# Performance work log

Hardware: AMD Instinct MI355X
Metric: run time of the kernel (lower is better)

Reference implementation:

```python
import jax, jax.numpy as jnp
import numpy as np

IN_DIM = 768
D_MODEL = 256
B, T = 64, 2048
LN_EPS = 1e-5


def setup_inputs() -> dict:
    key = jax.random.key(0)
    ks = jax.random.split(key, 8)
    s_in = 1.0 / np.sqrt(IN_DIM)
    s_d = 1.0 / np.sqrt(D_MODEL)
    return {
        "x": jax.random.normal(ks[0], (B, T, IN_DIM), dtype=jnp.float32),
        "ln_gamma": jnp.ones((IN_DIM,), jnp.float32),
        "ln_beta": jnp.zeros((IN_DIM,), jnp.float32),
        "W_proj": jax.random.uniform(ks[1], (IN_DIM, D_MODEL), jnp.float32, -s_in, s_in),
        "b_proj": jax.random.uniform(ks[2], (D_MODEL,), jnp.float32, -s_in, s_in),
        "W1": jax.random.uniform(ks[3], (D_MODEL, D_MODEL), jnp.float32, -s_d, s_d),
        "b1": jax.random.uniform(ks[4], (D_MODEL,), jnp.float32, -s_d, s_d),
        "W2": jax.random.uniform(ks[5], (D_MODEL,), jnp.float32, -s_d, s_d),
        "b2": jax.random.uniform(ks[6], (), jnp.float32, -s_d, s_d),
    }


def reference(x, ln_gamma, ln_beta, W_proj, b_proj, W1, b1, W2, b2):
    # nan/inf sanitization to 0
    x = jnp.nan_to_num(x, nan=0.0, posinf=0.0, neginf=0.0)
    # LayerNorm over last dim (biased variance, eps=1e-5)
    mu = jnp.mean(x, axis=-1, keepdims=True)
    var = jnp.mean(jnp.square(x - mu), axis=-1, keepdims=True)
    xn = (x - mu) * jax.lax.rsqrt(var + LN_EPS) * ln_gamma + ln_beta
    # projection to d_model: [B, T, D]
    h = jnp.einsum('btf,fd->btd', xn, W_proj) + b_proj
    # tanh-MLP attention scores: [B, T]
    a = jnp.tanh(jnp.einsum('btd,de->bte', h, W1) + b1)
    w = jnp.einsum('bte,e->bt', a, W2) + b2
    w = jax.nn.softmax(w, axis=-1)
    # weighted-sum pooling over T: [B, D]
    return jnp.einsum('btd,bt->bd', h, w)
```

## Files before the change

kernel.cpp:

```cpp
#include <hip/hip_runtime.h>

#define LN_EPS 1e-5f

typedef __attribute__((ext_vector_type(8))) short s8vec;
typedef __attribute__((ext_vector_type(4))) float f4vec;

#define OFF_WPT   0u
#define OFF_W1T   393216u
#define OFF_U     524288u
#define OFF_C     525312u
#define OFF_UPART 526336u
#define OFF_VPART 575488u
#define OFF_PM    624640u
#define OFF_PS    632832u
#define OFF_PO    641024u

__device__ __forceinline__ unsigned short f2bf(float f) {
  unsigned int u = __float_as_uint(f);
  u += 0x7fffu + ((u >> 16) & 1u);
  return (unsigned short)(u >> 16);
}
__device__ __forceinline__ float bf2f(unsigned short h) {
  return __uint_as_float(((unsigned int)h) << 16);
}
__device__ __forceinline__ void gll16(const void* g, void* l) {
  __builtin_amdgcn_global_load_lds(
      (const __attribute__((address_space(1))) unsigned int*)g,
      (__attribute__((address_space(3))) unsigned int*)l, 16, 0, 0);
}

__global__ void k0_prep(const float* __restrict__ Wp,
                        const float* __restrict__ gamma,
                        const float* __restrict__ beta,
                        const float* __restrict__ W1,
                        char* __restrict__ ws) {
  const int blk = blockIdx.x;
  const int n = threadIdx.x;
  const int sw = (n & 7) << 4;
  if (blk < 48) {
    unsigned short* wpt = (unsigned short*)(ws + OFF_WPT);
    const int k0 = blk * 16;
    float up = 0.f, vp = 0.f;
#pragma unroll
    for (int j = 0; j < 16; ++j) {
      const int k = k0 + j;
      const float w = Wp[k * 256 + n];
      const float wpv = gamma[k] * w;
      up += wpv;
      vp += beta[k] * w;
      const int c = k >> 6, kc = k & 63;
      wpt[c * 16384 + n * 64 + ((((kc * 2) ^ sw)) >> 1)] = f2bf(wpv);
    }
    ((float*)(ws + OFF_UPART))[blk * 256 + n] = up;
    ((float*)(ws + OFF_VPART))[blk * 256 + n] = vp;
  } else {
    unsigned short* w1t = (unsigned short*)(ws + OFF_W1T);
    const int d0 = (blk - 48) * 16;
#pragma unroll
    for (int j = 0; j < 16; ++j) {
      const int d = d0 + j;
      const int c = d >> 6, dc = d & 63;
      w1t[c * 16384 + n * 64 + ((((dc * 2) ^ sw)) >> 1)] = f2bf(W1[d * 256 + n]);
    }
  }
}

__global__ void k0_reduce(const float* __restrict__ bproj, char* __restrict__ ws) {
  const int n = threadIdx.x;
  const float* upart = (const float*)(ws + OFF_UPART);
  const float* vpart = (const float*)(ws + OFF_VPART);
  float u = 0.f, v = 0.f;
  for (int i = 0; i < 48; ++i) {
    u += upart[i * 256 + n];
    v += vpart[i * 256 + n];
  }
  ((float*)(ws + OFF_U))[n] = u;
  ((float*)(ws + OFF_C))[n] = v + bproj[n];
}

__global__ __launch_bounds__(256, 2)
void k1_main(const float* __restrict__ x,
             const float* __restrict__ b1,
             const float* __restrict__ W2,
             char* __restrict__ ws) {
  __shared__ __align__(16) char sm_h[32768];
  __shared__ __align__(16) char sm_b[32768];
  __shared__ __align__(16) char sm_a[8192];
  __shared__ float sm_u[256], sm_c[256], sm_b1[256], sm_w2[256];
  __shared__ float sm_mu[64], sm_inv[64];
  __shared__ float sm_lp[64 * 4];
  __shared__ float sm_lg[64];
  __shared__ float sm_e[64];

  const int tid  = threadIdx.x;
  const int lane = tid & 63;
  const int wid  = tid >> 6;
  const int lr = lane & 15;
  const int lq = lane >> 4;

  sm_u[tid]  = ((const float*)(ws + OFF_U))[tid];
  sm_c[tid]  = ((const float*)(ws + OFF_C))[tid];
  sm_b1[tid] = b1[tid];
  sm_w2[tid] = W2[tid];

  const int arow = tid >> 2;
  const int aq   = tid & 3;
  const float* xrow = x + (size_t)(blockIdx.x * 64 + arow) * 768 + aq * 16;

  const char* bsrc = (const char*)ws + OFF_WPT + wid * 8192 + lane * 16;
  char*       bdst = sm_b + wid * 8192 + lane * 16;

  const f4vec fz = {0.f, 0.f, 0.f, 0.f};
  f4vec acc[4][4];
#pragma unroll
  for (int m = 0; m < 4; ++m)
#pragma unroll
    for (int n = 0; n < 4; ++n) acc[m][n] = fz;

  float s1 = 0.f, s2 = 0.f;
  float4 va[4];
#pragma unroll
  for (int j = 0; j < 4; ++j) va[j] = *(const float4*)(xrow + j * 4);

  for (int c = 0; c < 12; ++c) {
#pragma unroll
    for (int s = 0; s < 8; ++s) gll16(bsrc + c * 32768 + s * 1024, bdst + s * 1024);
    float v[16];
#pragma unroll
    for (int j = 0; j < 4; ++j) {
      v[4*j+0] = va[j].x; v[4*j+1] = va[j].y; v[4*j+2] = va[j].z; v[4*j+3] = va[j].w;
    }
    unsigned int pk[8];
#pragma unroll
    for (int j = 0; j < 16; ++j) {
      float f = v[j];
      if ((__float_as_uint(f) & 0x7f800000u) == 0x7f800000u) f = 0.f;
      s1 += f; s2 += f * f;
      const unsigned int hb = f2bf(f);
      if ((j & 1) == 0) pk[j >> 1] = hb; else pk[j >> 1] |= hb << 16;
    }
    {
      const int base = arow * 128 + aq * 32;
      const int sw = (arow & 7) << 4;
      *(int4*)(sm_a + ((base     ) ^ sw)) = make_int4((int)pk[0], (int)pk[1], (int)pk[2], (int)pk[3]);
      *(int4*)(sm_a + ((base + 16) ^ sw)) = make_int4((int)pk[4], (int)pk[5], (int)pk[6], (int)pk[7]);
    }
    if (c < 11) {
#pragma unroll
      for (int j = 0; j < 4; ++j) va[j] = *(const float4*)(xrow + (c + 1) * 64 + j * 4);
    }
    __syncthreads();
#pragma unroll
    for (int ks = 0; ks < 2; ++ks) {
      const int kb = (ks * 32 + lq * 8) * 2;
      s8vec af[4], bfv[4];
#pragma unroll
      for (int m = 0; m < 4; ++m) {
        const int row = m * 16 + lr;
        af[m] = *(const s8vec*)(sm_a + ((row * 128 + kb) ^ ((row & 7) << 4)));
      }
#pragma unroll
      for (int n = 0; n < 4; ++n) {
        const int row = wid * 64 + n * 16 + lr;
        bfv[n] = *(const s8vec*)(sm_b + ((row * 128 + kb) ^ ((row & 7) << 4)));
      }
#pragma unroll
      for (int m = 0; m < 4; ++m)
#pragma unroll
        for (int n = 0; n < 4; ++n)
          acc[m][n] = __builtin_amdgcn_mfma_f32_16x16x32_bf16(af[m], bfv[n], acc[m][n], 0, 0, 0);
    }
    __syncthreads();
  }

  s1 += __shfl_xor(s1, 1); s1 += __shfl_xor(s1, 2);
  s2 += __shfl_xor(s2, 1); s2 += __shfl_xor(s2, 2);
  if (aq == 0) {
    const float mu = s1 * (1.f / 768.f);
    float var = s2 * (1.f / 768.f) - mu * mu;
    var = fmaxf(var, 0.f);
    sm_mu[arow]  = mu;
    sm_inv[arow] = rsqrtf(var + LN_EPS);
  }
  __syncthreads();

#pragma unroll
  for (int m = 0; m < 4; ++m) {
#pragma unroll
    for (int i = 0; i < 4; ++i) {
      const int rl = m * 16 + lq * 4 + i;
      const float mu  = sm_mu[rl];
      const float inv = sm_inv[rl];
      const int sw = (rl & 7) << 4;
#pragma unroll
      for (int n = 0; n < 4; ++n) {
        const int cd = wid * 64 + n * 16 + lr;
        const float h = inv * (acc[m][n][i] - mu * sm_u[cd]) + sm_c[cd];
        *(unsigned short*)(sm_h + ((rl * 512 + cd * 2) ^ sw)) = f2bf(h);
      }
    }
  }
  __syncthreads();

  f4vec acc2[4][4];
#pragma unroll
  for (int m = 0; m < 4; ++m)
#pragma unroll
    for (int n = 0; n < 4; ++n) acc2[m][n] = fz;

  const char* b2src = (const char*)ws + OFF_W1T + wid * 8192 + lane * 16;
  for (int c = 0; c < 4; ++c) {
#pragma unroll
    for (int s = 0; s < 8; ++s) gll16(b2src + c * 32768 + s * 1024, bdst + s * 1024);
    __syncthreads();
#pragma unroll
    for (int ks = 0; ks < 2; ++ks) {
      const int kh = (c * 64 + ks * 32 + lq * 8) * 2;
      const int kb = (ks * 32 + lq * 8) * 2;
      s8vec af[4], bfv[4];
#pragma unroll
      for (int m = 0; m < 4; ++m) {
        const int row = m * 16 + lr;
        af[m] = *(const s8vec*)(sm_h + ((row * 512 + kh) ^ ((row & 7) << 4)));
      }
#pragma unroll
      for (int n = 0; n < 4; ++n) {
        const int row = wid * 64 + n * 16 + lr;
        bfv[n] = *(const s8vec*)(sm_b + ((row * 128 + kb) ^ ((row & 7) << 4)));
      }
#pragma unroll
      for (int m = 0; m < 4; ++m)
#pragma unroll
        for (int n = 0; n < 4; ++n)
          acc2[m][n] = __builtin_amdgcn_mfma_f32_16x16x32_bf16(af[m], bfv[n], acc2[m][n], 0, 0, 0);
    }
    __syncthreads();
  }

  float lp[4][4];
#pragma unroll
  for (int m = 0; m < 4; ++m)
#pragma unroll
    for (int i = 0; i < 4; ++i) lp[m][i] = 0.f;

#pragma unroll
  for (int m = 0; m < 4; ++m) {
#pragma unroll
    for (int n = 0; n < 4; ++n) {
      const int cd = wid * 64 + n * 16 + lr;
      const float b1v = sm_b1[cd];
      const float w2v = sm_w2[cd];
#pragma unroll
      for (int i = 0; i < 4; ++i) {
        float z = acc2[m][n][i] + b1v;
        z = fminf(fmaxf(z, -15.f), 15.f);
        const float e2 = __expf(2.f * z);
        const float a = (e2 - 1.f) / (e2 + 1.f);
        lp[m][i] += a * w2v;
      }
    }
  }
#pragma unroll
  for (int m = 0; m < 4; ++m) {
#pragma unroll
    for (int i = 0; i < 4; ++i) {
      float t = lp[m][i];
      t += __shfl_xor(t, 1);
      t += __shfl_xor(t, 2);
      t += __shfl_xor(t, 4);
      t += __shfl_xor(t, 8);
      if (lr == 0) sm_lp[(m * 16 + lq * 4 + i) * 4 + wid] = t;
    }
  }
  __syncthreads();
  if (tid < 64)
    sm_lg[tid] = sm_lp[tid*4+0] + sm_lp[tid*4+1] + sm_lp[tid*4+2] + sm_lp[tid*4+3];
  __syncthreads();

  float mx = -1e30f;
  for (int r = 0; r < 64; ++r) mx = fmaxf(mx, sm_lg[r]);
  if (tid < 64) sm_e[tid] = __expf(sm_lg[tid] - mx);
  __syncthreads();

  {
    const int d = tid;
    float o = 0.f;
    for (int r = 0; r < 64; ++r) {
      const float ev = sm_e[r];
      const unsigned short hb =
          *(const unsigned short*)(sm_h + ((r * 512 + d * 2) ^ ((r & 7) << 4)));
      o += ev * bf2f(hb);
    }
    ((float*)(ws + OFF_PO))[blockIdx.x * 256 + d] = o;
  }
  if (tid == 0) {
    float s = 0.f;
    for (int r = 0; r < 64; ++r) s += sm_e[r];
    ((float*)(ws + OFF_PS))[blockIdx.x] = s;
    ((float*)(ws + OFF_PM))[blockIdx.x] = mx;
  }
}

__global__ void k2_combine(const char* __restrict__ ws, float* __restrict__ out) {
  const int b = blockIdx.x;
  const int d = threadIdx.x;
  const float* pm = (const float*)(ws + OFF_PM) + b * 32;
  const float* ps = (const float*)(ws + OFF_PS) + b * 32;
  const float* po = (const float*)(ws + OFF_PO) + (size_t)b * 32 * 256;
  float mx = -1e30f;
  for (int c = 0; c < 32; ++c) mx = fmaxf(mx, pm[c]);
  float num = 0.f, den = 0.f;
  for (int c = 0; c < 32; ++c) {
    const float al = __expf(pm[c] - mx);
    den += al * ps[c];
    num += al * po[c * 256 + d];
  }
  out[b * 256 + d] = num / den;
}

extern "C" void kernel_launch(void* const* d_in, const int* in_sizes, int n_in,
                              void* d_out, int out_size, void* d_ws, size_t ws_size,
                              hipStream_t stream) {
  const float* x     = (const float*)d_in[0];
  const float* gamma = (const float*)d_in[1];
  const float* beta  = (const float*)d_in[2];
  const float* Wp    = (const float*)d_in[3];
  const float* bproj = (const float*)d_in[4];
  const float* W1    = (const float*)d_in[5];
  const float* b1    = (const float*)d_in[6];
  const float* W2    = (const float*)d_in[7];
  char* ws = (char*)d_ws;
  float* out = (float*)d_out;

  k0_prep   <<<dim3(64),   dim3(256), 0, stream>>>(Wp, gamma, beta, W1, ws);
  k0_reduce <<<dim3(1),    dim3(256), 0, stream>>>(bproj, ws);
  k1_main   <<<dim3(2048), dim3(256), 0, stream>>>(x, b1, W2, ws);
  k2_combine<<<dim3(64),   dim3(256), 0, stream>>>(ws, out);
}
```

Baseline: 173.3 us.

## Pipeline global loads with manual waitcnt barriers and double-buffered x prefetch

Replaces __syncthreads with explicit s_waitcnt/s_barrier so the vector-memory counter can stay partially outstanding. The x row prefetch now runs two chunks ahead using alternating register buffers. The first W1 chunk load is issued during the LayerNorm epilogue, and later W1 chunks are loaded while the MFMAs of the current chunk run, after the fragments have been read into registers. This hides global-load latency behind compute, but depends on hand-counted vmcnt values, which are fragile if the compiler reorders or adds memory ops.

```diff
diff --git a/kernel.cpp b/kernel.cpp
--- a/kernel.cpp
+++ b/kernel.cpp
@@ -14,6 +14,13 @@
 #define OFF_PM    624640u
 #define OFF_PS    632832u
 #define OFF_PO    641024u
+
+#define BAR()     asm volatile("s_barrier" ::: "memory")
+#define WAIT_V4() asm volatile("s_waitcnt vmcnt(4) lgkmcnt(0)" ::: "memory")
+#define WAIT_V0() asm volatile("s_waitcnt vmcnt(0) lgkmcnt(0)" ::: "memory")
+#define WAIT_L0() asm volatile("s_waitcnt lgkmcnt(0)" ::: "memory")
+#define ORDER_FENCE() do { asm volatile("" ::: "memory"); \
+                           __builtin_amdgcn_sched_barrier(0); } while (0)
 
 __device__ __forceinline__ unsigned short f2bf(float f) {
   unsigned int u = __float_as_uint(f);
@@ -107,8 +114,9 @@
   const int aq   = tid & 3;
   const float* xrow = x + (size_t)(blockIdx.x * 64 + arow) * 768 + aq * 16;
 
-  const char* bsrc = (const char*)ws + OFF_WPT + wid * 8192 + lane * 16;
-  char*       bdst = sm_b + wid * 8192 + lane * 16;
+  const char* bsrc  = (const char*)ws + OFF_WPT + wid * 8192 + lane * 16;
+  const char* b2src = (const char*)ws + OFF_W1T + wid * 8192 + lane * 16;
+  char*       bdst  = sm_b + wid * 8192 + lane * 16;
 
   const f4vec fz = {0.f, 0.f, 0.f, 0.f};
   f4vec acc[4][4];
@@ -118,13 +126,16 @@
     for (int n = 0; n < 4; ++n) acc[m][n] = fz;
 
   float s1 = 0.f, s2 = 0.f;
-  float4 va[4];
-#pragma unroll
-  for (int j = 0; j < 4; ++j) va[j] = *(const float4*)(xrow + j * 4);
-
-  for (int c = 0; c < 12; ++c) {
+  float4 vaA[4], vaB[4];
+#pragma unroll
+  for (int j = 0; j < 4; ++j) vaA[j] = *(const float4*)(xrow + 0 * 64 + j * 4);
+#pragma unroll
+  for (int j = 0; j < 4; ++j) vaB[j] = *(const float4*)(xrow + 1 * 64 + j * 4);
+
+  auto p1body = [&](int c, float4 (&va)[4], bool pf) {
 #pragma unroll
     for (int s = 0; s < 8; ++s) gll16(bsrc + c * 32768 + s * 1024, bdst + s * 1024);
+    ORDER_FENCE();
     float v[16];
 #pragma unroll
     for (int j = 0; j < 4; ++j) {
@@ -145,11 +156,12 @@
       *(int4*)(sm_a + ((base     ) ^ sw)) = make_int4((int)pk[0], (int)pk[1], (int)pk[2], (int)pk[3]);
       *(int4*)(sm_a + ((base + 16) ^ sw)) = make_int4((int)pk[4], (int)pk[5], (int)pk[6], (int)pk[7]);
     }
-    if (c < 11) {
-#pragma unroll
-      for (int j = 0; j < 4; ++j) va[j] = *(const float4*)(xrow + (c + 1) * 64 + j * 4);
-    }
-    __syncthreads();
+    if (pf) {
+#pragma unroll
+      for (int j = 0; j < 4; ++j) va[j] = *(const float4*)(xrow + (c + 2) * 64 + j * 4);
+    }
+    if (pf) WAIT_V4(); else WAIT_V0();
+    BAR();
 #pragma unroll
     for (int ks = 0; ks < 2; ++ks) {
       const int kb = (ks * 32 + lq * 8) * 2;
@@ -170,7 +182,12 @@
         for (int n = 0; n < 4; ++n)
           acc[m][n] = __builtin_amdgcn_mfma_f32_16x16x32_bf16(af[m], bfv[n], acc[m][n], 0, 0, 0);
     }
-    __syncthreads();
+    BAR();
+  };
+
+  for (int cc = 0; cc < 12; cc += 2) {
+    p1body(cc,     vaA, cc + 2 < 12);
+    p1body(cc + 1, vaB, cc + 3 < 12);
   }
 
   s1 += __shfl_xor(s1, 1); s1 += __shfl_xor(s1, 2);
@@ -182,7 +199,10 @@
     sm_mu[arow]  = mu;
     sm_inv[arow] = rsqrtf(var + LN_EPS);
   }
-  __syncthreads();
+#pragma unroll
+  for (int s = 0; s < 8; ++s) gll16(b2src + s * 1024, bdst + s * 1024);
+  WAIT_L0();
+  BAR();
 
 #pragma unroll
   for (int m = 0; m < 4; ++m) {
@@ -200,7 +220,8 @@
       }
     }
   }
-  __syncthreads();
+  WAIT_V0();
+  BAR();
 
   f4vec acc2[4][4];
 #pragma unroll
@@ -208,33 +229,38 @@
 #pragma unroll
     for (int n = 0; n < 4; ++n) acc2[m][n] = fz;
 
-  const char* b2src = (const char*)ws + OFF_W1T + wid * 8192 + lane * 16;
   for (int c = 0; c < 4; ++c) {
-#pragma unroll
-    for (int s = 0; s < 8; ++s) gll16(b2src + c * 32768 + s * 1024, bdst + s * 1024);
-    __syncthreads();
+    s8vec af[2][4], bfv[2][4];
 #pragma unroll
     for (int ks = 0; ks < 2; ++ks) {
       const int kh = (c * 64 + ks * 32 + lq * 8) * 2;
       const int kb = (ks * 32 + lq * 8) * 2;
-      s8vec af[4], bfv[4];
 #pragma unroll
       for (int m = 0; m < 4; ++m) {
         const int row = m * 16 + lr;
-        af[m] = *(const s8vec*)(sm_h + ((row * 512 + kh) ^ ((row & 7) << 4)));
+        af[ks][m] = *(const s8vec*)(sm_h + ((row * 512 + kh) ^ ((row & 7) << 4)));
       }
 #pragma unroll
       for (int n = 0; n < 4; ++n) {
         const int row = wid * 64 + n * 16 + lr;
-        bfv[n] = *(const s8vec*)(sm_b + ((row * 128 + kb) ^ ((row & 7) << 4)));
-      }
+        bfv[ks][n] = *(const s8vec*)(sm_b + ((row * 128 + kb) ^ ((row & 7) << 4)));
+      }
+    }
+    WAIT_L0();
+    BAR();
+    if (c < 3) {
+#pragma unroll
+      for (int s = 0; s < 8; ++s) gll16(b2src + (c + 1) * 32768 + s * 1024, bdst + s * 1024);
+    }
+#pragma unroll
+    for (int ks = 0; ks < 2; ++ks)
 #pragma unroll
       for (int m = 0; m < 4; ++m)
 #pragma unroll
         for (int n = 0; n < 4; ++n)
-          acc2[m][n] = __builtin_amdgcn_mfma_f32_16x16x32_bf16(af[m], bfv[n], acc2[m][n], 0, 0, 0);
-    }
-    __syncthreads();
+          acc2[m][n] = __builtin_amdgcn_mfma_f32_16x16x32_bf16(af[ks][m], bfv[ks][n], acc2[m][n], 0, 0, 0);
+    if (c < 3) WAIT_V0();
+    BAR();
   }
 
   float lp[4][4];
```

Result: no change. 170.4 us (-1.7%).

## Split fused projection/MLP kernel into two kernels with h staged in global memory

Applied to the files above, without the earlier changes.

The single fused kernel is split into a projection kernel and an MLP/pooling kernel. The projection kernel gives each wave 16 rows across all 256 output columns, builds A fragments straight from registers instead of through LDS, and replaces __syncthreads with hand-placed waitcnt and barrier instructions. It writes bf16 h to a new global workspace region. The second kernel reads h and a plain row-major W1^T directly from global memory without LDS staging. This raises occupancy and removes LDS round trips, at the cost of an extra global write and read of h (about 64 MB) and one more kernel launch.

```diff
diff --git a/kernel.cpp b/kernel.cpp
--- a/kernel.cpp
+++ b/kernel.cpp
@@ -14,6 +14,14 @@
 #define OFF_PM    624640u
 #define OFF_PS    632832u
 #define OFF_PO    641024u
+#define OFF_H     3145728u
+
+#define BAR()     asm volatile("s_barrier" ::: "memory")
+#define WAIT_V4() asm volatile("s_waitcnt vmcnt(4) lgkmcnt(0)" ::: "memory")
+#define WAIT_V0() asm volatile("s_waitcnt vmcnt(0) lgkmcnt(0)" ::: "memory")
+#define WAIT_L0() asm volatile("s_waitcnt lgkmcnt(0)" ::: "memory")
+#define ORDER_FENCE() do { asm volatile("" ::: "memory"); \
+                           __builtin_amdgcn_sched_barrier(0); } while (0)
 
 __device__ __forceinline__ unsigned short f2bf(float f) {
   unsigned int u = __float_as_uint(f);
@@ -59,8 +67,7 @@
 #pragma unroll
     for (int j = 0; j < 16; ++j) {
       const int d = d0 + j;
-      const int c = d >> 6, dc = d & 63;
-      w1t[c * 16384 + n * 64 + ((((dc * 2) ^ sw)) >> 1)] = f2bf(W1[d * 256 + n]);
+      w1t[n * 256 + d] = f2bf(W1[d * 256 + n]);
     }
   }
 }
@@ -78,19 +85,11 @@
   ((float*)(ws + OFF_C))[n] = v + bproj[n];
 }
 
-__global__ __launch_bounds__(256, 2)
-void k1_main(const float* __restrict__ x,
-             const float* __restrict__ b1,
-             const float* __restrict__ W2,
-             char* __restrict__ ws) {
-  __shared__ __align__(16) char sm_h[32768];
+__global__ __launch_bounds__(256, 3)
+void k1a_proj(const float* __restrict__ x, char* __restrict__ ws) {
   __shared__ __align__(16) char sm_b[32768];
-  __shared__ __align__(16) char sm_a[8192];
-  __shared__ float sm_u[256], sm_c[256], sm_b1[256], sm_w2[256];
+  __shared__ float sm_u[256], sm_c[256];
   __shared__ float sm_mu[64], sm_inv[64];
-  __shared__ float sm_lp[64 * 4];
-  __shared__ float sm_lg[64];
-  __shared__ float sm_e[64];
 
   const int tid  = threadIdx.x;
   const int lane = tid & 63;
@@ -98,165 +97,173 @@
   const int lr = lane & 15;
   const int lq = lane >> 4;
 
-  sm_u[tid]  = ((const float*)(ws + OFF_U))[tid];
-  sm_c[tid]  = ((const float*)(ws + OFF_C))[tid];
-  sm_b1[tid] = b1[tid];
-  sm_w2[tid] = W2[tid];
-
-  const int arow = tid >> 2;
-  const int aq   = tid & 3;
-  const float* xrow = x + (size_t)(blockIdx.x * 64 + arow) * 768 + aq * 16;
-
+  sm_u[tid] = ((const float*)(ws + OFF_U))[tid];
+  sm_c[tid] = ((const float*)(ws + OFF_C))[tid];
+
+  const float* xrow = x + (size_t)(blockIdx.x * 64 + wid * 16 + lr) * 768 + lq * 8;
   const char* bsrc = (const char*)ws + OFF_WPT + wid * 8192 + lane * 16;
   char*       bdst = sm_b + wid * 8192 + lane * 16;
 
   const f4vec fz = {0.f, 0.f, 0.f, 0.f};
-  f4vec acc[4][4];
-#pragma unroll
-  for (int m = 0; m < 4; ++m)
-#pragma unroll
-    for (int n = 0; n < 4; ++n) acc[m][n] = fz;
+  f4vec acc[16];
+#pragma unroll
+  for (int n = 0; n < 16; ++n) acc[n] = fz;
 
   float s1 = 0.f, s2 = 0.f;
-  float4 va[4];
-#pragma unroll
-  for (int j = 0; j < 4; ++j) va[j] = *(const float4*)(xrow + j * 4);
+  float4 xc[4];
+#pragma unroll
+  for (int q = 0; q < 4; ++q)
+    xc[q] = *(const float4*)(xrow + (q >> 1) * 32 + (q & 1) * 4);
 
   for (int c = 0; c < 12; ++c) {
 #pragma unroll
     for (int s = 0; s < 8; ++s) gll16(bsrc + c * 32768 + s * 1024, bdst + s * 1024);
-    float v[16];
-#pragma unroll
-    for (int j = 0; j < 4; ++j) {
-      v[4*j+0] = va[j].x; v[4*j+1] = va[j].y; v[4*j+2] = va[j].z; v[4*j+3] = va[j].w;
-    }
-    unsigned int pk[8];
-#pragma unroll
-    for (int j = 0; j < 16; ++j) {
-      float f = v[j];
-      if ((__float_as_uint(f) & 0x7f800000u) == 0x7f800000u) f = 0.f;
-      s1 += f; s2 += f * f;
-      const unsigned int hb = f2bf(f);
-      if ((j & 1) == 0) pk[j >> 1] = hb; else pk[j >> 1] |= hb << 16;
-    }
-    {
-      const int base = arow * 128 + aq * 32;
-      const int sw = (arow & 7) << 4;
-      *(int4*)(sm_a + ((base     ) ^ sw)) = make_int4((int)pk[0], (int)pk[1], (int)pk[2], (int)pk[3]);
-      *(int4*)(sm_a + ((base + 16) ^ sw)) = make_int4((int)pk[4], (int)pk[5], (int)pk[6], (int)pk[7]);
+    ORDER_FENCE();
+    s8vec af[2];
+#pragma unroll
+    for (int ks = 0; ks < 2; ++ks) {
+      float v[8];
+#pragma unroll
+      for (int j = 0; j < 4; ++j) { v[j] = ((const float*)&xc[ks*2])[j];
+                                    v[4+j] = ((const float*)&xc[ks*2+1])[j]; }
+      unsigned int pk[4];
+#pragma unroll
+      for (int j = 0; j < 8; ++j) {
+        float f = v[j];
+        if ((__float_as_uint(f) & 0x7f800000u) == 0x7f800000u) f = 0.f;
+        s1 += f; s2 += f * f;
+        const unsigned int hb = f2bf(f);
+        if ((j & 1) == 0) pk[j >> 1] = hb; else pk[j >> 1] |= hb << 16;
+      }
+      af[ks] = *(s8vec*)pk;
     }
     if (c < 11) {
 #pragma unroll
-      for (int j = 0; j < 4; ++j) va[j] = *(const float4*)(xrow + (c + 1) * 64 + j * 4);
-    }
-    __syncthreads();
+      for (int q = 0; q < 4; ++q)
+        xc[q] = *(const float4*)(xrow + (c + 1) * 64 + (q >> 1) * 32 + (q & 1) * 4);
+    }
+    if (c < 11) WAIT_V4(); else WAIT_V0();
+    BAR();
 #pragma unroll
     for (int ks = 0; ks < 2; ++ks) {
       const int kb = (ks * 32 + lq * 8) * 2;
-      s8vec af[4], bfv[4];
-#pragma unroll
-      for (int m = 0; m < 4; ++m) {
-        const int row = m * 16 + lr;
-        af[m] = *(const s8vec*)(sm_a + ((row * 128 + kb) ^ ((row & 7) << 4)));
+#pragma unroll
+      for (int n = 0; n < 16; ++n) {
+        const int row = n * 16 + lr;
+        const s8vec bf = *(const s8vec*)(sm_b + ((row * 128 + kb) ^ ((row & 7) << 4)));
+        acc[n] = __builtin_amdgcn_mfma_f32_16x16x32_bf16(af[ks], bf, acc[n], 0, 0, 0);
       }
-#pragma unroll
-      for (int n = 0; n < 4; ++n) {
-        const int row = wid * 64 + n * 16 + lr;
-        bfv[n] = *(const s8vec*)(sm_b + ((row * 128 + kb) ^ ((row & 7) << 4)));
-      }
-#pragma unroll
-      for (int m = 0; m < 4; ++m)
-#pragma unroll
-        for (int n = 0; n < 4; ++n)
-          acc[m][n] = __builtin_amdgcn_mfma_f32_16x16x32_bf16(af[m], bfv[n], acc[m][n], 0, 0, 0);
-    }
-    __syncthreads();
-  }
-
-  s1 += __shfl_xor(s1, 1); s1 += __shfl_xor(s1, 2);
-  s2 += __shfl_xor(s2, 1); s2 += __shfl_xor(s2, 2);
-  if (aq == 0) {
+    }
+    BAR();
+  }
+
+  s1 += __shfl_xor(s1, 16); s1 += __shfl_xor(s1, 32);
+  s2 += __shfl_xor(s2, 16); s2 += __shfl_xor(s2, 32);
+  {
     const float mu = s1 * (1.f / 768.f);
     float var = s2 * (1.f / 768.f) - mu * mu;
     var = fmaxf(var, 0.f);
-    sm_mu[arow]  = mu;
-    sm_inv[arow] = rsqrtf(var + LN_EPS);
-  }
-  __syncthreads();
+    if (lane < 16) {
+      sm_mu[wid * 16 + lr]  = mu;
+      sm_inv[wid * 16 + lr] = rsqrtf(var + LN_EPS);
+    }
+  }
+  WAIT_L0();
+
+  unsigned int* hout = (unsigned int*)(ws + OFF_H) + (size_t)blockIdx.x * 64 * 128;
+  const int odd = lane & 1;
+  float muv[4], invv[4];
+#pragma unroll
+  for (int i = 0; i < 4; ++i) {
+    muv[i]  = sm_mu[wid * 16 + lq * 4 + i];
+    invv[i] = sm_inv[wid * 16 + lq * 4 + i];
+  }
+#pragma unroll
+  for (int n = 0; n < 16; ++n) {
+    const int cd = n * 16 + lr;
+    const float uv = sm_u[cd], cv = sm_c[cd];
+    float hv[4];
+#pragma unroll
+    for (int i = 0; i < 4; ++i)
+      hv[i] = invv[i] * (acc[n][i] - muv[i] * uv) + cv;
+#pragma unroll
+    for (int i = 0; i < 4; ++i) {
+      const float hp = __shfl_xor(hv[i], 1);
+      if ((i >> 1) == odd) {
+        const unsigned int lo = odd ? f2bf(hp) : f2bf(hv[i]);
+        const unsigned int hi = odd ? f2bf(hv[i]) : f2bf(hp);
+        hout[(wid * 16 + lq * 4 + i) * 128 + n * 8 + (lr >> 1)] = lo | (hi << 16);
+      }
+    }
+  }
+}
+
+__global__ __launch_bounds__(256, 3)
+void k1b_mlp(const float* __restrict__ b1,
+             const float* __restrict__ W2,
+             char* __restrict__ ws) {
+  __shared__ float sm_lp[64 * 4];
+  __shared__ float sm_lg[64];
+  __shared__ float sm_e[64];
+
+  const int tid  = threadIdx.x;
+  const int lane = tid & 63;
+  const int wid  = tid >> 6;
+  const int lr = lane & 15;
+  const int lq = lane >> 4;
+
+  const unsigned short* hb  = (const unsigned short*)(ws + OFF_H) +
+                              (size_t)blockIdx.x * 64 * 256;
+  const unsigned short* w1t = (const unsigned short*)(ws + OFF_W1T);
+
+  float b1v[4], w2v[4];
+#pragma unroll
+  for (int n = 0; n < 4; ++n) {
+    const int e = wid * 64 + n * 16 + lr;
+    b1v[n] = b1[e]; w2v[n] = W2[e];
+  }
+
+  const f4vec fz = {0.f, 0.f, 0.f, 0.f};
+  f4vec acc2[4][4];
+#pragma unroll
+  for (int m = 0; m < 4; ++m)
+#pragma unroll
+    for (int n = 0; n < 4; ++n) acc2[m][n] = fz;
+
+#pragma unroll
+  for (int ks = 0; ks < 8; ++ks) {
+    s8vec af[4], bf[4];
+#pragma unroll
+    for (int m = 0; m < 4; ++m)
+      af[m] = *(const s8vec*)(hb + (m * 16 + lr) * 256 + ks * 32 + lq * 8);
+#pragma unroll
+    for (int n = 0; n < 4; ++n)
+      bf[n] = *(const s8vec*)(w1t + (wid * 64 + n * 16 + lr) * 256 + ks * 32 + lq * 8);
+#pragma unroll
+    for (int m = 0; m < 4; ++m)
+#pragma unroll
+      for (int n = 0; n < 4; ++n)
+        acc2[m][n] = __builtin_amdgcn_mfma_f32_16x16x32_bf16(af[m], bf[n], acc2[m][n], 0, 0, 0);
+  }
+
+  float lp[4][4];
+#pragma unroll
+  for (int m = 0; m < 4; ++m)
+#pragma unroll
+    for (int i = 0; i < 4; ++i) lp[m][i] = 0.f;
 
 #pragma unroll
   for (int m = 0; m < 4; ++m) {
 #pragma unroll
-    for (int i = 0; i < 4; ++i) {
-      const int rl = m * 16 + lq * 4 + i;
-      const float mu  = sm_mu[rl];
-      const float inv = sm_inv[rl];
-      const int sw = (rl & 7) << 4;
-#pragma unroll
-      for (int n = 0; n < 4; ++n) {
-        const int cd = wid * 64 + n * 16 + lr;
-        const float h = inv * (acc[m][n][i] - mu * sm_u[cd]) + sm_c[cd];
-        *(unsigned short*)(sm_h + ((rl * 512 + cd * 2) ^ sw)) = f2bf(h);
-      }
-    }
-  }
-  __syncthreads();
-
-  f4vec acc2[4][4];
-#pragma unroll
-  for (int m = 0; m < 4; ++m)
-#pragma unroll
-    for (int n = 0; n < 4; ++n) acc2[m][n] = fz;
-
-  const char* b2src = (const char*)ws + OFF_W1T + wid * 8192 + lane * 16;
-  for (int c = 0; c < 4; ++c) {
-#pragma unroll
-    for (int s = 0; s < 8; ++s) gll16(b2src + c * 32768 + s * 1024, bdst + s * 1024);
-    __syncthreads();
-#pragma unroll
-    for (int ks = 0; ks < 2; ++ks) {
-      const int kh = (c * 64 + ks * 32 + lq * 8) * 2;
-      const int kb = (ks * 32 + lq * 8) * 2;
-      s8vec af[4], bfv[4];
-#pragma unroll
-      for (int m = 0; m < 4; ++m) {
-        const int row = m * 16 + lr;
-        af[m] = *(const s8vec*)(sm_h + ((row * 512 + kh) ^ ((row & 7) << 4)));
-      }
-#pragma unroll
-      for (int n = 0; n < 4; ++n) {
-        const int row = wid * 64 + n * 16 + lr;
-        bfv[n] = *(const s8vec*)(sm_b + ((row * 128 + kb) ^ ((row & 7) << 4)));
-      }
-#pragma unroll
-      for (int m = 0; m < 4; ++m)
-#pragma unroll
-        for (int n = 0; n < 4; ++n)
-          acc2[m][n] = __builtin_amdgcn_mfma_f32_16x16x32_bf16(af[m], bfv[n], acc2[m][n], 0, 0, 0);
-    }
-    __syncthreads();
-  }
-
-  float lp[4][4];
-#pragma unroll
-  for (int m = 0; m < 4; ++m)
-#pragma unroll
-    for (int i = 0; i < 4; ++i) lp[m][i] = 0.f;
-
-#pragma unroll
-  for (int m = 0; m < 4; ++m) {
-#pragma unroll
     for (int n = 0; n < 4; ++n) {
-      const int cd = wid * 64 + n * 16 + lr;
-      const float b1v = sm_b1[cd];
-      const float w2v = sm_w2[cd];
+      const float b1n = b1v[n], w2n = w2v[n];
 #pragma unroll
       for (int i = 0; i < 4; ++i) {
-        float z = acc2[m][n][i] + b1v;
+        float z = acc2[m][n][i] + b1n;
         z = fminf(fmaxf(z, -15.f), 15.f);
         const float e2 = __expf(2.f * z);
         const float a = (e2 - 1.f) / (e2 + 1.f);
-        lp[m][i] += a * w2v;
+        lp[m][i] += a * w2n;
       }
     }
   }
@@ -283,15 +290,10 @@
   __syncthreads();
 
   {
-    const int d = tid;
     float o = 0.f;
-    for (int r = 0; r < 64; ++r) {
-      const float ev = sm_e[r];
-      const unsigned short hb =
-          *(const unsigned short*)(sm_h + ((r * 512 + d * 2) ^ ((r & 7) << 4)));
-      o += ev * bf2f(hb);
-    }
-    ((float*)(ws + OFF_PO))[blockIdx.x * 256 + d] = o;
+    for (int r = 0; r < 64; ++r)
+      o += sm_e[r] * bf2f(hb[r * 256 + tid]);
+    ((float*)(ws + OFF_PO))[blockIdx.x * 256 + tid] = o;
   }
   if (tid == 0) {
     float s = 0.f;
@@ -334,6 +336,7 @@
 
   k0_prep   <<<dim3(64),   dim3(256), 0, stream>>>(Wp, gamma, beta, W1, ws);
   k0_reduce <<<dim3(1),    dim3(256), 0, stream>>>(bproj, ws);
-  k1_main   <<<dim3(2048), dim3(256), 0, stream>>>(x, b1, W2, ws);
+  k1a_proj  <<<dim3(2048), dim3(256), 0, stream>>>(x, ws);
+  k1b_mlp   <<<dim3(2048), dim3(256), 0, stream>>>(b1, W2, ws);
   k2_combine<<<dim3(64),   dim3(256), 0, stream>>>(ws, out);
 }
```

New measurement: 213.6 us. 23.2% more time.
